# Performance work log

Hardware: AMD Instinct MI355X
Metric: run time of the kernel (lower is better)

The kernel has to match this reference:

```python
import jax, jax.numpy as jnp
import numpy as np

N_CELLS, N_GENES = 10000, 4000
CELL_F, GENE_F = 2000, 50
HID, LAT, NCLUST = 256, 64, 20
N_EDGES = 640000
ALPHA = 1.0


def _lin(key, fan_in, fan_out):
    k1, k2 = jax.random.split(key)
    bound = 1.0 / np.sqrt(fan_in)
    w = jax.random.uniform(k1, (fan_in, fan_out), jnp.float32, -bound, bound)
    b = jax.random.uniform(k2, (fan_out,), jnp.float32, -bound, bound)
    return w, b


def setup_inputs() -> dict:
    key = jax.random.key(0)
    ks = jax.random.split(key, 20)
    inp = {
        'cell_x': jax.random.normal(ks[0], (N_CELLS, CELL_F), jnp.float32),
        'gene_x': jax.random.normal(ks[1], (N_GENES, GENE_F), jnp.float32),
        'edge_row': jax.random.randint(ks[2], (N_EDGES,), 0, N_CELLS),
        'edge_col': jax.random.randint(ks[3], (N_EDGES,), 0, N_GENES),
        'edge_val': jax.random.uniform(ks[4], (N_EDGES,), jnp.float32),
    }
    # layer 0: cell_in=CELL_F, gene_in=GENE_F -> HID
    inp['l0_cs_w'], inp['l0_cs_b'] = _lin(ks[5], CELL_F, HID)
    inp['l0_cn_w'], inp['l0_cn_b'] = _lin(ks[6], GENE_F, HID)
    inp['l0_gs_w'], inp['l0_gs_b'] = _lin(ks[7], GENE_F, HID)
    inp['l0_gn_w'], inp['l0_gn_b'] = _lin(ks[8], CELL_F, HID)
    # layer 1: HID -> HID
    inp['l1_cs_w'], inp['l1_cs_b'] = _lin(ks[9], HID, HID)
    inp['l1_cn_w'], inp['l1_cn_b'] = _lin(ks[10], HID, HID)
    inp['l1_gs_w'], inp['l1_gs_b'] = _lin(ks[11], HID, HID)
    inp['l1_gn_w'], inp['l1_gn_b'] = _lin(ks[12], HID, HID)
    # latent heads and decoders
    inp['cl_w'], inp['cl_b'] = _lin(ks[13], HID, LAT)
    inp['gl_w'], inp['gl_b'] = _lin(ks[14], HID, LAT)
    inp['cd_w'], inp['cd_b'] = _lin(ks[15], LAT, N_GENES)
    inp['gd_w'], inp['gd_b'] = _lin(ks[16], LAT, N_CELLS)
    inp['centers'] = jax.random.normal(ks[17], (NCLUST, LAT), jnp.float32)
    return inp


def _bip_conv(cell_x, gene_x, er, ec, ev,
              cs_w, cs_b, cn_w, cn_b, gs_w, gs_b, gn_w, gn_b):
    # sparse adjacency matmul as gather + segment_sum over edge list
    cell_neigh = jax.ops.segment_sum(ev[:, None] * gene_x[ec], er,
                                     num_segments=cell_x.shape[0])
    gene_neigh = jax.ops.segment_sum(ev[:, None] * cell_x[er], ec,
                                     num_segments=gene_x.shape[0])
    cell_out = jax.nn.relu(cell_x @ cs_w + cs_b + cell_neigh @ cn_w + cn_b)
    gene_out = jax.nn.relu(gene_x @ gs_w + gs_b + gene_neigh @ gn_w + gn_b)
    return cell_out, gene_out


def reference(cell_x, gene_x, edge_row, edge_col, edge_val,
              l0_cs_w, l0_cs_b, l0_cn_w, l0_cn_b, l0_gs_w, l0_gs_b, l0_gn_w, l0_gn_b,
              l1_cs_w, l1_cs_b, l1_cn_w, l1_cn_b, l1_gs_w, l1_gs_b, l1_gn_w, l1_gn_b,
              cl_w, cl_b, gl_w, gl_b, cd_w, cd_b, gd_w, gd_b, centers):
    c, g = _bip_conv(cell_x, gene_x, edge_row, edge_col, edge_val,
                     l0_cs_w, l0_cs_b, l0_cn_w, l0_cn_b,
                     l0_gs_w, l0_gs_b, l0_gn_w, l0_gn_b)
    c, g = _bip_conv(c, g, edge_row, edge_col, edge_val,
                     l1_cs_w, l1_cs_b, l1_cn_w, l1_cn_b,
                     l1_gs_w, l1_gs_b, l1_gn_w, l1_gn_b)
    z_cells = c @ cl_w + cl_b
    z_genes = g @ gl_w + gl_b
    cell_recon = z_cells @ cd_w + cd_b
    gene_recon = z_genes @ gd_w + gd_b
    # Student-t cluster assignment (DEC)
    sq_dist = jnp.sum((z_cells[:, None, :] - centers[None, :, :]) ** 2, axis=-1)
    numerator = (1.0 + sq_dist / ALPHA) ** (-(ALPHA + 1.0) / 2.0)
    q = numerator / jnp.sum(numerator, axis=1, keepdims=True)
    return z_cells, z_genes, cell_recon, gene_recon, q
```

## Files before the change

kernel.cpp:

```cpp
#include <hip/hip_runtime.h>

#define N_CELLS 10000
#define N_GENES 4000
#define CELL_F  2000
#define CELL_FX 2112
#define GENE_F  50
#define GENE_FP 64
#define HID     256
#define LAT     64
#define NCLUST  20
#define N_EDGES 640000

typedef __attribute__((ext_vector_type(8))) short    bf16x8;
typedef __attribute__((ext_vector_type(8))) unsigned short u16x8;
typedef __attribute__((ext_vector_type(4))) float    f32x4;

__device__ __forceinline__ unsigned short f2bf(float f) {
    unsigned int u = __float_as_uint(f);
    unsigned int r = (u + 0x7FFFu + ((u >> 16) & 1u)) >> 16;
    return (unsigned short)r;
}
__device__ __forceinline__ float bf2f(unsigned short h) {
    return __uint_as_float(((unsigned int)h) << 16);
}

#define GLOAD_LDS16(gp, lp) __builtin_amdgcn_global_load_lds( \
    (const __attribute__((address_space(1))) void*)(gp), \
    (__attribute__((address_space(3))) void*)(lp), 16, 0, 0)

struct GemmDesc {
    const unsigned short *A, *BT;
    const float *bias;
    float *C;
    unsigned short *Cbf;
    int M, N, K;
    int gx, nwg, blk0;
    const float *bias2;
    unsigned short *Cbf2;
};
struct GemmArgs2 { GemmDesc d[2]; };
struct ScatArgs {
    const int *er, *ec; const float *ev;
    int *cur_c, *cur_g;
    int *ci; float *cv; int *gi; float *gv;
};

template<int TM, bool BIAS, bool WF32, bool WBF, bool TEPI, bool QTAIL, bool SCAT, bool RSPLIT>
__global__ __launch_bounds__(256)
void gemm_multi(GemmArgs2 ga, int gemm0, int qstart,
                const float* __restrict__ zq, const float* __restrict__ cent,
                float* __restrict__ qout, ScatArgs sa)
{
    constexpr int SMEM = (TM * 128 + 8192) > 16640 ? (TM * 128 + 8192) : 16640;
    __shared__ __align__(16) unsigned char smem[SMEM];
    unsigned short* As = (unsigned short*)smem;
    unsigned short* Bs = As + TM * 64;

    if (SCAT && (int)blockIdx.x < gemm0) {
        int e = blockIdx.x * 256 + threadIdx.x;
        int r = sa.er[e], c = sa.ec[e];
        float v = sa.ev[e];
        int pc = atomicAdd(&sa.cur_c[r], 1);
        sa.ci[pc] = c; sa.cv[pc] = v;
        int pg = atomicAdd(&sa.cur_g[c], 1);
        sa.gi[pg] = r; sa.gv[pg] = v;
        return;
    }

    if (QTAIL && (int)blockIdx.x >= qstart) {
        float* cs = (float*)smem;
        int tid = threadIdx.x;
        for (int l = tid; l < NCLUST * LAT; l += 256) cs[l] = cent[l];
        __syncthreads();
        int c = (blockIdx.x - qstart) * 256 + tid;
        if (c >= N_CELLS) return;
        float zr[LAT];
        #pragma unroll
        for (int k = 0; k < LAT; ++k) zr[k] = zq[(size_t)c * LAT + k];
        float num[NCLUST];
        float denom = 0.0f;
        for (int j = 0; j < NCLUST; ++j) {
            float d = 0.0f;
            #pragma unroll
            for (int k = 0; k < LAT; ++k) {
                float t = zr[k] - cs[j * LAT + k];
                d += t * t;
            }
            float n = 1.0f / (1.0f + d);
            num[j] = n;
            denom += n;
        }
        float inv = 1.0f / denom;
        for (int j = 0; j < NCLUST; ++j) qout[(size_t)c * NCLUST + j] = num[j] * inv;
        return;
    }

    int b = blockIdx.x;
    int p = (b >= ga.d[1].blk0) ? 1 : 0;
    const GemmDesc d = ga.d[p];
    int lin = b - d.blk0;
    int q8 = d.nwg >> 3, r8 = d.nwg & 7;
    int xcd = lin & 7, idx = lin >> 3;
    int wgid = (xcd < r8 ? xcd * (q8 + 1) : r8 * (q8 + 1) + (xcd - r8) * q8) + idx;
    int by = wgid / d.gx;
    int bx = wgid - by * d.gx;

    const int tid  = threadIdx.x;
    const int lane = tid & 63;
    const int w    = tid >> 6;
    const int cn   = lane & 15;
    const int rj   = lane >> 4;
    const int row0 = by * TM;
    const int col0 = bx * 64;

    constexpr int AI = TM / 32;
    constexpr int MF = TM / 64;

    size_t arow[AI];
    unsigned short* ldsA[AI];
    #pragma unroll
    for (int j = 0; j < AI; ++j) {
        int slot = (w * AI + j) * 64 + lane;
        int rs = slot >> 3, ss = slot & 7, cs = ss ^ (rs & 7);
        arow[j] = (size_t)min(row0 + rs, d.M - 1) * d.K + cs * 8;
        ldsA[j] = As + (w * AI + j) * 512;
    }
    const int sb0 = (w * 2) * 64 + lane;
    const int sb1 = sb0 + 64;
    const int rb0 = sb0 >> 3, cb0 = (sb0 & 7) ^ (rb0 & 7);
    const int rb1 = sb1 >> 3, cb1 = (sb1 & 7) ^ (rb1 & 7);
    const size_t brow0 = (size_t)(col0 + rb0) * d.K + cb0 * 8;
    const size_t brow1 = (size_t)(col0 + rb1) * d.K + cb1 * 8;
    unsigned short* ldsB = Bs + (w * 2) * 512;

    int aoff0[MF], aoff1[MF];
    #pragma unroll
    for (int mf = 0; mf < MF; ++mf) {
        int rA = w * (TM / 4) + mf * 16 + cn, swA = rA & 7, abase = rA * 64;
        aoff0[mf] = abase + ((rj)     ^ swA) * 8;
        aoff1[mf] = abase + ((rj + 4) ^ swA) * 8;
    }

    f32x4 acc[MF][4] = {};

    for (int kt = 0; kt < d.K; kt += 64) {
        #pragma unroll
        for (int j = 0; j < AI; ++j) GLOAD_LDS16(d.A + arow[j] + kt, ldsA[j]);
        GLOAD_LDS16(d.BT + brow0 + kt, ldsB);
        GLOAD_LDS16(d.BT + brow1 + kt, ldsB + 512);
        __syncthreads();
        bf16x8 a0[MF], a1[MF];
        #pragma unroll
        for (int mf = 0; mf < MF; ++mf) {
            a0[mf] = *(const bf16x8*)&As[aoff0[mf]];
            a1[mf] = *(const bf16x8*)&As[aoff1[mf]];
        }
        #pragma unroll
        for (int f = 0; f < 4; ++f) {
            int rB = f * 16 + cn, swB = rB & 7, bb = rB * 64;
            bf16x8 b0 = *(const bf16x8*)&Bs[bb + ((rj)     ^ swB) * 8];
            bf16x8 b1 = *(const bf16x8*)&Bs[bb + ((rj + 4) ^ swB) * 8];
            #pragma unroll
            for (int mf = 0; mf < MF; ++mf) {
                acc[mf][f] = __builtin_amdgcn_mfma_f32_16x16x32_bf16(a0[mf], b0, acc[mf][f], 0, 0, 0);
                acc[mf][f] = __builtin_amdgcn_mfma_f32_16x16x32_bf16(a1[mf], b1, acc[mf][f], 0, 0, 0);
            }
        }
        __syncthreads();
    }

    if (TEPI) {
        float* Cs = (float*)smem;
        __syncthreads();
        #pragma unroll
        for (int f = 0; f < 4; ++f)
            #pragma unroll
            for (int j = 0; j < 4; ++j)
                Cs[(w * 16 + rj * 4 + j) * 65 + f * 16 + cn] = acc[0][f][j];
        __syncthreads();
        #pragma unroll
        for (int i = 0; i < 4; ++i) {
            int slot = tid + i * 256;
            int rr = slot >> 4, c4 = (slot & 15) * 4;
            int gr = row0 + rr, gc = col0 + c4;
            if (gr < d.M && gc < d.N) {
                const float* cp = &Cs[rr * 65 + c4];
                float4 bv = BIAS ? *(const float4*)&d.bias[gc] : float4{0, 0, 0, 0};
                float4 v;
                v.x = cp[0] + bv.x; v.y = cp[1] + bv.y;
                v.z = cp[2] + bv.z; v.w = cp[3] + bv.w;
                *(float4*)&d.C[(size_t)gr * d.N + gc] = v;
            }
        }
    } else if (RSPLIT) {
        #pragma unroll
        for (int mf = 0; mf < MF; ++mf) {
            #pragma unroll
            for (int f = 0; f < 4; ++f) {
                int col = col0 + f * 16 + cn;
                #pragma unroll
                for (int j = 0; j < 4; ++j) {
                    int r = row0 + w * (TM / 4) + mf * 16 + rj * 4 + j;
                    if (r < d.M) {
                        float val = acc[mf][f][j];
                        if (col < 256) {
                            val += d.bias[col] + d.bias2[col];
                            d.Cbf[(size_t)r * 256 + col] = f2bf(fmaxf(val, 0.0f));
                        } else {
                            d.Cbf2[(size_t)r * 256 + (col - 256)] = f2bf(val);
                        }
                    }
                }
            }
        }
    } else {
        #pragma unroll
        for (int mf = 0; mf < MF; ++mf) {
            #pragma unroll
            for (int f = 0; f < 4; ++f) {
                int col = col0 + f * 16 + cn;
                if (col >= d.N) continue;
                float bv = BIAS ? d.bias[col] : 0.0f;
                #pragma unroll
                for (int j = 0; j < 4; ++j) {
                    int r = row0 + w * (TM / 4) + mf * 16 + rj * 4 + j;
                    if (r < d.M) {
                        float val = acc[mf][f][j] + bv;
                        if (WF32) d.C[(size_t)r * d.N + col] = val;
                        if (WBF)  d.Cbf[(size_t)r * d.N + col] = f2bf(val);
                    }
                }
            }
        }
    }
}

__global__ __launch_bounds__(256)
void rawgather_kernel(const int* __restrict__ ptr, const int* __restrict__ nbr,
                      const float* __restrict__ val,
                      const unsigned short* __restrict__ gx,
                      unsigned short* __restrict__ cellx)
{
    int w = threadIdx.x >> 6, lane = threadIdx.x & 63;
    int r = blockIdx.x * 4 + w;
    int s = ptr[r], e = ptr[r + 1];
    int g = lane >> 4, sub = lane & 15;
    const ushort4* gx4 = (const ushort4*)gx;
    float4 acc = {0.0f, 0.0f, 0.0f, 0.0f};
    for (int base = s; base < e; base += 16) {
        int nb = 0; float vb = 0.0f;
        if (lane < 16 && base + lane < e) { nb = nbr[base + lane]; vb = val[base + lane]; }
        #pragma unroll
        for (int jj = 0; jj < 4; ++jj) {
            int ei = jj * 4 + g;
            int j  = __shfl(nb, ei);
            float v = __shfl(vb, ei);
            ushort4 a = gx4[(size_t)j * 16 + sub];
            acc.x += v * bf2f(a.x);
            acc.y += v * bf2f(a.y);
            acc.z += v * bf2f(a.z);
            acc.w += v * bf2f(a.w);
        }
    }
    acc.x += __shfl_xor(acc.x, 16); acc.x += __shfl_xor(acc.x, 32);
    acc.y += __shfl_xor(acc.y, 16); acc.y += __shfl_xor(acc.y, 32);
    acc.z += __shfl_xor(acc.z, 16); acc.z += __shfl_xor(acc.z, 32);
    acc.w += __shfl_xor(acc.w, 16); acc.w += __shfl_xor(acc.w, 32);
    if (lane < 16) {
        ushort4 o;
        o.x = f2bf(acc.x); o.y = f2bf(acc.y); o.z = f2bf(acc.z); o.w = f2bf(acc.w);
        ((ushort4*)(cellx + (size_t)r * CELL_FX + 2048))[sub] = o;
    }
}

struct PackDesc {
    const float* W1; const float* W2; const float* W3; unsigned short* BT;
    int Kr, Kp, N1, N2, Np, xb, blk0;
};
struct PackArgs { PackDesc d[8]; };

#define CNT_BLK   2500
#define CVTC_BLK  10000
#define CVTG_BLK  125
#define PACK_BLK0 (CNT_BLK + CVTC_BLK + CVTG_BLK)

__global__ __launch_bounds__(256)
void prep_kernel(const int* __restrict__ er, const int* __restrict__ ec,
                 int* __restrict__ cnt_c, int* __restrict__ cnt_g,
                 const float* __restrict__ cell_x, unsigned short* __restrict__ cellx_bf,
                 const float* __restrict__ gene_x, unsigned short* __restrict__ genex_bf,
                 PackArgs pa)
{
    __shared__ float tile[32][33];
    int b = blockIdx.x;
    int tid = threadIdx.x;
    if (b < CNT_BLK) {
        int e = b * 256 + tid;
        atomicAdd(&cnt_c[er[e]], 1);
        atomicAdd(&cnt_g[ec[e]], 1);
        return;
    }
    if (b < CNT_BLK + CVTC_BLK) {
        int row = b - CNT_BLK;
        int col = tid * 8;
        u16x8 v = {0, 0, 0, 0, 0, 0, 0, 0};
        if (col < CELL_F) {
            const float* src = cell_x + (size_t)row * CELL_F + col;
            float4 f0 = *(const float4*)src;
            float4 f1 = *(const float4*)(src + 4);
            v[0] = f2bf(f0.x); v[1] = f2bf(f0.y); v[2] = f2bf(f0.z); v[3] = f2bf(f0.w);
            v[4] = f2bf(f1.x); v[5] = f2bf(f1.y); v[6] = f2bf(f1.z); v[7] = f2bf(f1.w);
        }
        ((u16x8*)(cellx_bf + (size_t)row * CELL_FX))[tid] = v;
        return;
    }
    if (b < PACK_BLK0) {
        int idx = (b - CNT_BLK - CVTC_BLK) * 256 + tid;
        int row = idx >> 3, c8 = idx & 7;
        int col = c8 * 8;
        u16x8 v = {0, 0, 0, 0, 0, 0, 0, 0};
        #pragma unroll
        for (int j = 0; j < 8; ++j)
            if (col + j < GENE_F) v[j] = f2bf(gene_x[(size_t)row * GENE_F + col + j]);
        ((u16x8*)(genex_bf + (size_t)row * GENE_FP))[c8] = v;
        return;
    }
    int pb = b;
    int p = 0;
    #pragma unroll
    for (int i = 1; i < 8; ++i) if (pb >= pa.d[i].blk0) p = i;
    const PackDesc d = pa.d[p];
    int local = pb - d.blk0;
    int kb = local % d.xb, nb = local / d.xb;
    int k0 = kb * 32, n0 = nb * 32;
    int tx = tid & 31, ty = tid >> 5;
    #pragma unroll
    for (int yy = 0; yy < 4; ++yy) {
        int k = k0 + ty + yy * 8;
        int n = n0 + tx;
        float v = 0.0f;
        if (k < d.Kr) {
            if (n < d.N1) v = d.W1[(size_t)k * d.N1 + n];
            else if (n < d.N1 + d.N2) v = d.W2[(size_t)k * d.N2 + (n - d.N1)];
        } else if (d.W3 && k >= 2048) {
            int kk = k - 2048;
            if (kk < GENE_F && n < HID) v = d.W3[(size_t)kk * HID + n];
        }
        tile[ty + yy * 8][tx] = v;
    }
    __syncthreads();
    #pragma unroll
    for (int yy = 0; yy < 4; ++yy) {
        int n = n0 + ty + yy * 8;
        int k = k0 + tx;
        if (n < d.Np)
            d.BT[(size_t)n * d.Kp + k] = f2bf(tile[tx][ty + yy * 8]);
    }
}

__global__ __launch_bounds__(1024)
void scan2_kernel(const int* __restrict__ cnt_c, int* __restrict__ ptr_c, int* __restrict__ cur_c,
                  const int* __restrict__ cnt_g, int* __restrict__ ptr_g, int* __restrict__ cur_g)
{
    const int* cnt = blockIdx.x ? cnt_g : cnt_c;
    int* ptr = blockIdx.x ? ptr_g : ptr_c;
    int* cur = blockIdx.x ? cur_g : cur_c;
    int  n   = blockIdx.x ? N_GENES : N_CELLS;
    __shared__ int part[1024];
    int t = threadIdx.x;
    int chunk = (n + 1023) / 1024;
    int lo = t * chunk, hi = min(lo + chunk, n);
    int s = 0;
    for (int i = lo; i < hi; ++i) s += cnt[i];
    part[t] = s;
    __syncthreads();
    #pragma unroll
    for (int off = 1; off < 1024; off <<= 1) {
        int v = (t >= off) ? part[t - off] : 0;
        __syncthreads();
        part[t] += v;
        __syncthreads();
    }
    if (t == 1023) ptr[n] = part[1023];
    int run = part[t] - s;
    for (int i = lo; i < hi; ++i) { ptr[i] = run; cur[i] = run; run += cnt[i]; }
}

struct AggSide {
    const int *ptr, *nbr; const float *val;
    const unsigned short *src, *pre;
    const float *b1, *b2;
    unsigned short *out;
    int srcRow4, srcOff4, preRow;
};
struct AggArgs { AggSide s[2]; int nc; };

__global__ __launch_bounds__(256)
void agg2_kernel(AggArgs aa)
{
    __shared__ __align__(16) float red[4][256];
    int b = blockIdx.x;
    int side = (b >= aa.nc) ? 1 : 0;
    const AggSide S = aa.s[side];
    int r = side ? b - aa.nc : b;
    int t = threadIdx.x;
    int w = t >> 6;
    int lane = t & 63;
    int s = S.ptr[r], e = S.ptr[r + 1];
    int n = e - s;
    int chunk = (n + 3) >> 2;
    int ws = s + w * chunk;
    int we = min(ws + chunk, e);
    const ushort4* src4 = (const ushort4*)S.src;
    float4 acc = {0.0f, 0.0f, 0.0f, 0.0f};
    for (int base = ws; base < we; base += 16) {
        int   nb = 0;
        float vb = 0.0f;
        if (lane < 16 && base + lane < we) {
            nb = S.nbr[base + lane];
            vb = S.val[base + lane];
        }
        #pragma unroll
        for (int j = 0; j < 16; ++j) {
            int   jj = __shfl(nb, j);
            float vv = __shfl(vb, j);
            ushort4 a = src4[(size_t)jj * S.srcRow4 + S.srcOff4 + lane];
            acc.x += vv * bf2f(a.x);
            acc.y += vv * bf2f(a.y);
            acc.z += vv * bf2f(a.z);
            acc.w += vv * bf2f(a.w);
        }
    }
    *(float4*)&red[w][lane * 4] = acc;
    __syncthreads();
    float x = red[0][t] + red[1][t] + red[2][t] + red[3][t]
            + bf2f(S.pre[(size_t)r * S.preRow + t]) + S.b1[t] + S.b2[t];
    S.out[(size_t)r * 256 + t] = f2bf(fmaxf(x, 0.0f));
}

extern "C" void kernel_launch(void* const* d_in, const int* in_sizes, int n_in,
                              void* d_out, int out_size, void* d_ws, size_t ws_size,
                              hipStream_t stream)
{
    const float* cell_x  = (const float*)d_in[0];
    const float* gene_x  = (const float*)d_in[1];
    const int*   er      = (const int*)d_in[2];
    const int*   ec      = (const int*)d_in[3];
    const float* ev      = (const float*)d_in[4];
    const float* l0_cs_w = (const float*)d_in[5];  const float* l0_cs_b = (const float*)d_in[6];
    const float* l0_cn_w = (const float*)d_in[7];  const float* l0_cn_b = (const float*)d_in[8];
    const float* l0_gs_w = (const float*)d_in[9];  const float* l0_gs_b = (const float*)d_in[10];
    const float* l0_gn_w = (const float*)d_in[11]; const float* l0_gn_b = (const float*)d_in[12];
    const float* l1_cs_w = (const float*)d_in[13]; const float* l1_cs_b = (const float*)d_in[14];
    const float* l1_cn_w = (const float*)d_in[15]; const float* l1_cn_b = (const float*)d_in[16];
    const float* l1_gs_w = (const float*)d_in[17]; const float* l1_gs_b = (const float*)d_in[18];
    const float* l1_gn_w = (const float*)d_in[19]; const float* l1_gn_b = (const float*)d_in[20];
    const float* cl_w = (const float*)d_in[21]; const float* cl_b = (const float*)d_in[22];
    const float* gl_w = (const float*)d_in[23]; const float* gl_b = (const float*)d_in[24];
    const float* cd_w = (const float*)d_in[25]; const float* cd_b = (const float*)d_in[26];
    const float* gd_w = (const float*)d_in[27]; const float* gd_b = (const float*)d_in[28];
    const float* centers = (const float*)d_in[29];

    float* out = (float*)d_out;
    float* z_cells    = out;
    float* z_genes    = out + 640000;
    float* cell_recon = out + 896000;
    float* gene_recon = out + 40896000;
    float* q          = out + 80896000;

    char* wsp = (char*)d_ws;
    auto alloc = [&](size_t bytes) -> void* {
        void* p = (void*)wsp;
        wsp += (bytes + 255) & ~(size_t)255;
        return p;
    };
    unsigned short* pre_c_bf = (unsigned short*)alloc((size_t)N_CELLS * 512 * 2);
    unsigned short* pre_g_bf = (unsigned short*)alloc((size_t)N_GENES * 512 * 2);
    unsigned short* c1_bf    = (unsigned short*)alloc((size_t)N_CELLS * 256 * 2);
    unsigned short* g1_bf    = (unsigned short*)alloc((size_t)N_GENES * 256 * 2);
    unsigned short* c2_bf    = (unsigned short*)alloc((size_t)N_CELLS * 256 * 2);
    unsigned short* g2_bf    = (unsigned short*)alloc((size_t)N_GENES * 256 * 2);
    unsigned short* zc_bf    = (unsigned short*)alloc((size_t)N_CELLS * 64 * 2);
    unsigned short* zg_bf    = (unsigned short*)alloc((size_t)N_GENES * 64 * 2);
    unsigned short* cellx_bf = (unsigned short*)alloc((size_t)N_CELLS * CELL_FX * 2);
    unsigned short* genex_bf = (unsigned short*)alloc((size_t)N_GENES * GENE_FP * 2);
    unsigned short* W0cT = (unsigned short*)alloc((size_t)512 * CELL_FX * 2);
    unsigned short* W0gT = (unsigned short*)alloc((size_t)256 * GENE_FP * 2);
    unsigned short* W1cT = (unsigned short*)alloc((size_t)512 * HID * 2);
    unsigned short* W1gT = (unsigned short*)alloc((size_t)512 * HID * 2);
    unsigned short* WzcT = (unsigned short*)alloc((size_t)64 * HID * 2);
    unsigned short* WzgT = (unsigned short*)alloc((size_t)64 * HID * 2);
    unsigned short* WdcT = (unsigned short*)alloc((size_t)4032 * 64 * 2);
    unsigned short* WdgT = (unsigned short*)alloc((size_t)10048 * 64 * 2);
    int* cnt_c = (int*)alloc((size_t)(N_CELLS + N_GENES) * 4);
    int* cnt_g = cnt_c + N_CELLS;
    int* ptr_c = (int*)alloc((size_t)(N_CELLS + 1) * 4);
    int* ptr_g = (int*)alloc((size_t)(N_GENES + 1) * 4);
    int* cur_c = (int*)alloc((size_t)N_CELLS * 4);
    int* cur_g = (int*)alloc((size_t)N_GENES * 4);
    int*   ci = (int*)alloc((size_t)N_EDGES * 4);
    float* cv = (float*)alloc((size_t)N_EDGES * 4);
    int*   gi = (int*)alloc((size_t)N_EDGES * 4);
    float* gv = (float*)alloc((size_t)N_EDGES * 4);
    unsigned short* pre_cgn_bf = c2_bf;
    unsigned short* pre_gs_bf  = g2_bf;

    hipMemsetAsync(cnt_c, 0, (size_t)(N_CELLS + N_GENES) * 4, stream);

    {
        PackArgs pa;
        auto set = [&](int i, const float* W1, const float* W2, const float* W3,
                       unsigned short* BT, int Kr, int Kp, int N1, int N2, int Np,
                       int blk0) -> int {
            int xb = Kp / 32, yb = Np / 32;
            pa.d[i] = {W1, W2, W3, BT, Kr, Kp, N1, N2, Np, xb, blk0};
            return blk0 + xb * yb;
        };
        int nb = PACK_BLK0;
        nb = set(0, l0_cs_w, l0_gn_w, l0_cn_w, W0cT, CELL_F, CELL_FX, HID, HID, 512, nb);
        nb = set(1, l0_gs_w, nullptr, nullptr, W0gT, GENE_F, GENE_FP, HID, 0, 256, nb);
        nb = set(2, l1_cs_w, l1_gn_w, nullptr, W1cT, HID, HID, HID, HID, 512, nb);
        nb = set(3, l1_gs_w, l1_cn_w, nullptr, W1gT, HID, HID, HID, HID, 512, nb);
        nb = set(4, cl_w, nullptr, nullptr, WzcT, HID, HID, LAT, 0, 64, nb);
        nb = set(5, gl_w, nullptr, nullptr, WzgT, HID, HID, LAT, 0, 64, nb);
        nb = set(6, cd_w, nullptr, nullptr, WdcT, LAT, LAT, N_GENES, 0, 4032, nb);
        nb = set(7, gd_w, nullptr, nullptr, WdgT, LAT, LAT, N_CELLS, 0, 10048, nb);
        prep_kernel<<<nb, 256, 0, stream>>>(er, ec, cnt_c, cnt_g,
                                            cell_x, cellx_bf, gene_x, genex_bf, pa);
    }

    scan2_kernel<<<2, 1024, 0, stream>>>(cnt_c, ptr_c, cur_c, cnt_g, ptr_g, cur_g);

    auto mkdesc = [](const unsigned short* A, const unsigned short* BT, const float* bias,
                     float* C, unsigned short* Cbf, int M, int N, int K, int TMv,
                     int blk0) -> GemmDesc {
        int gx = (N + 63) / 64, gy = (M + TMv - 1) / TMv;
        return {A, BT, bias, C, Cbf, M, N, K, gx, gx * gy, blk0, nullptr, nullptr};
    };
    ScatArgs sa0 = {er, ec, ev, cur_c, cur_g, ci, cv, gi, gv};
    ScatArgs saN = {};

    {
        GemmArgs2 ga;
        ga.d[0] = mkdesc(genex_bf, W0gT, nullptr, nullptr, pre_gs_bf, N_GENES, 256, GENE_FP, 128, CNT_BLK);
        ga.d[1] = ga.d[0]; ga.d[1].blk0 = 1 << 30;
        gemm_multi<128, false, false, true, false, false, true, false>
            <<<CNT_BLK + ga.d[0].nwg, 256, 0, stream>>>(
            ga, CNT_BLK, 1 << 30, nullptr, nullptr, nullptr, sa0);
    }

    rawgather_kernel<<<N_CELLS / 4, 256, 0, stream>>>(ptr_c, ci, cv, genex_bf, cellx_bf);

    {
        GemmArgs2 ga;
        ga.d[0] = mkdesc(cellx_bf, W0cT, l0_cs_b, nullptr, c1_bf, N_CELLS, 512, CELL_FX, 128, 0);
        ga.d[0].bias2 = l0_cn_b;
        ga.d[0].Cbf2  = pre_cgn_bf;
        ga.d[1] = ga.d[0]; ga.d[1].blk0 = 1 << 30;
        gemm_multi<128, false, false, false, false, false, false, true>
            <<<ga.d[0].nwg, 256, 0, stream>>>(
            ga, 0, 1 << 30, nullptr, nullptr, nullptr, saN);
    }

    {
        AggArgs aa;
        aa.nc = 0;
        aa.s[1] = {ptr_g, gi, gv, pre_cgn_bf, pre_gs_bf, l0_gs_b, l0_gn_b, g1_bf, 64, 0, 256};
        aa.s[0] = aa.s[1];
        agg2_kernel<<<N_GENES, 256, 0, stream>>>(aa);
    }

    {
        GemmArgs2 ga;
        ga.d[0] = mkdesc(c1_bf, W1cT, nullptr, nullptr, pre_c_bf, N_CELLS, 512, HID, 128, 0);
        ga.d[1] = mkdesc(g1_bf, W1gT, nullptr, nullptr, pre_g_bf, N_GENES, 512, HID, 128,
                         ga.d[0].nwg);
        gemm_multi<128, false, false, true, false, false, false, false>
            <<<ga.d[1].blk0 + ga.d[1].nwg, 256, 0, stream>>>(
            ga, 0, 1 << 30, nullptr, nullptr, nullptr, saN);
    }

    {
        AggArgs aa;
        aa.nc = N_CELLS;
        aa.s[0] = {ptr_c, ci, cv, pre_g_bf, pre_c_bf, l1_cs_b, l1_cn_b, c2_bf, 128, 64, 512};
        aa.s[1] = {ptr_g, gi, gv, pre_c_bf, pre_g_bf, l1_gs_b, l1_gn_b, g2_bf, 128, 64, 512};
        agg2_kernel<<<N_CELLS + N_GENES, 256, 0, stream>>>(aa);
    }

    {
        GemmArgs2 ga;
        ga.d[0] = mkdesc(c2_bf, WzcT, cl_b, z_cells, zc_bf, N_CELLS, LAT, HID, 64, 0);
        ga.d[1] = mkdesc(g2_bf, WzgT, gl_b, z_genes, zg_bf, N_GENES, LAT, HID, 64, ga.d[0].nwg);
        gemm_multi<64, true, true, true, false, false, false, false>
            <<<ga.d[1].blk0 + ga.d[1].nwg, 256, 0, stream>>>(
            ga, 0, 1 << 30, nullptr, nullptr, nullptr, saN);
    }

    {
        GemmArgs2 ga;
        ga.d[0] = mkdesc(zc_bf, WdcT, cd_b, cell_recon, nullptr, N_CELLS, N_GENES, LAT, 64, 0);
        ga.d[1] = mkdesc(zg_bf, WdgT, gd_b, gene_recon, nullptr, N_GENES, N_CELLS, LAT, 64,
                         ga.d[0].nwg);
        int qstart = ga.d[1].blk0 + ga.d[1].nwg;
        int qblocks = (N_CELLS + 255) / 256;
        gemm_multi<64, true, true, false, true, true, false, false>
            <<<qstart + qblocks, 256, 0, stream>>>(
            ga, 0, qstart, z_cells, centers, q, saN);
    }
}
```

Before: 436.4 us.

## Aggregate raw layer-1 features before GEMM and fuse self/neighbor weights along K

Layer 1 now aggregates the raw hidden features into the second half of a concatenated [h | neighbor-sum] buffer. It then runs one GEMM with K=512 against stacked self and neighbor weights, with bias and ReLU fused into the epilogue. Before, it projected features to a 512-wide output first and aggregated the projected half afterwards. This removes the separate read of the precomputed self term in the aggregation and halves the GEMM output width. In exchange the GEMM reads a wider A matrix, and neighbor sums are rounded to bf16 before the matmul rather than after.

Measured after the change: 421.2 us (median of 2 runs). 1.04x faster.

```diff
diff --git a/kernel.cpp b/kernel.cpp
--- a/kernel.cpp
+++ b/kernel.cpp
@@ -37,6 +37,7 @@
     int gx, nwg, blk0;
     const float *bias2;
     unsigned short *Cbf2;
+    int ld1, ld2;
 };
 struct GemmArgs2 { GemmDesc d[2]; };
 struct ScatArgs {
@@ -198,6 +199,7 @@
             #pragma unroll
             for (int f = 0; f < 4; ++f) {
                 int col = col0 + f * 16 + cn;
+                if (col >= d.N) continue;
                 #pragma unroll
                 for (int j = 0; j < 4; ++j) {
                     int r = row0 + w * (TM / 4) + mf * 16 + rj * 4 + j;
@@ -205,9 +207,9 @@
                         float val = acc[mf][f][j];
                         if (col < 256) {
                             val += d.bias[col] + d.bias2[col];
-                            d.Cbf[(size_t)r * 256 + col] = f2bf(fmaxf(val, 0.0f));
+                            d.Cbf[(size_t)r * d.ld1 + col] = f2bf(fmaxf(val, 0.0f));
                         } else {
-                            d.Cbf2[(size_t)r * 256 + (col - 256)] = f2bf(val);
+                            d.Cbf2[(size_t)r * d.ld2 + (col - 256)] = f2bf(val);
                         }
                     }
                 }
@@ -275,7 +277,7 @@
 
 struct PackDesc {
     const float* W1; const float* W2; const float* W3; unsigned short* BT;
-    int Kr, Kp, N1, N2, Np, xb, blk0;
+    int Kr, Kp, N1, N2, Np, xb, blk0, kcat;
 };
 struct PackArgs { PackDesc d[8]; };
 
@@ -339,7 +341,11 @@
         int k = k0 + ty + yy * 8;
         int n = n0 + tx;
         float v = 0.0f;
-        if (k < d.Kr) {
+        if (d.kcat) {
+            if (n < d.Np)
+                v = (k < 256) ? d.W1[(size_t)k * d.N1 + n]
+                              : d.W2[(size_t)(k - 256) * d.N1 + n];
+        } else if (k < d.Kr) {
             if (n < d.N1) v = d.W1[(size_t)k * d.N1 + n];
             else if (n < d.N1 + d.N2) v = d.W2[(size_t)k * d.N2 + (n - d.N1)];
         } else if (d.W3 && k >= 2048) {
@@ -391,18 +397,14 @@
     const unsigned short *src, *pre;
     const float *b1, *b2;
     unsigned short *out;
-    int srcRow4, srcOff4, preRow;
+    int srcRow4, srcOff4, preRow, outLd;
 };
-struct AggArgs { AggSide s[2]; int nc; };
 
 __global__ __launch_bounds__(256)
-void agg2_kernel(AggArgs aa)
+void agg1_kernel(AggSide S)
 {
     __shared__ __align__(16) float red[4][256];
-    int b = blockIdx.x;
-    int side = (b >= aa.nc) ? 1 : 0;
-    const AggSide S = aa.s[side];
-    int r = side ? b - aa.nc : b;
+    int r = blockIdx.x;
     int t = threadIdx.x;
     int w = t >> 6;
     int lane = t & 63;
@@ -435,7 +437,57 @@
     __syncthreads();
     float x = red[0][t] + red[1][t] + red[2][t] + red[3][t]
             + bf2f(S.pre[(size_t)r * S.preRow + t]) + S.b1[t] + S.b2[t];
-    S.out[(size_t)r * 256 + t] = f2bf(fmaxf(x, 0.0f));
+    S.out[(size_t)r * S.outLd + t] = f2bf(fmaxf(x, 0.0f));
+}
+
+struct NsSide {
+    const int *ptr, *nbr; const float *val;
+    const unsigned short *src;
+    unsigned short *out;
+    int srcRow4, srcOff4, outLd, outOff;
+};
+struct NsArgs { NsSide s[2]; int n0; };
+
+__global__ __launch_bounds__(256)
+void neighsum_kernel(NsArgs na)
+{
+    __shared__ __align__(16) float red[4][256];
+    int b = blockIdx.x;
+    int side = (b >= na.n0) ? 1 : 0;
+    const NsSide S = na.s[side];
+    int r = side ? b - na.n0 : b;
+    int t = threadIdx.x;
+    int w = t >> 6;
+    int lane = t & 63;
+    int s = S.ptr[r], e = S.ptr[r + 1];
+    int n = e - s;
+    int chunk = (n + 3) >> 2;
+    int ws = s + w * chunk;
+    int we = min(ws + chunk, e);
+    const ushort4* src4 = (const ushort4*)S.src;
+    float4 acc = {0.0f, 0.0f, 0.0f, 0.0f};
+    for (int base = ws; base < we; base += 16) {
+        int   nb = 0;
+        float vb = 0.0f;
+        if (lane < 16 && base + lane < we) {
+            nb = S.nbr[base + lane];
+            vb = S.val[base + lane];
+        }
+        #pragma unroll
+        for (int j = 0; j < 16; ++j) {
+            int   jj = __shfl(nb, j);
+            float vv = __shfl(vb, j);
+            ushort4 a = src4[(size_t)jj * S.srcRow4 + S.srcOff4 + lane];
+            acc.x += vv * bf2f(a.x);
+            acc.y += vv * bf2f(a.y);
+            acc.z += vv * bf2f(a.z);
+            acc.w += vv * bf2f(a.w);
+        }
+    }
+    *(float4*)&red[w][lane * 4] = acc;
+    __syncthreads();
+    float x = red[0][t] + red[1][t] + red[2][t] + red[3][t];
+    S.out[(size_t)r * S.outLd + S.outOff + t] = f2bf(x);
 }
 
 extern "C" void kernel_launch(void* const* d_in, const int* in_sizes, int n_in,
@@ -474,10 +526,10 @@
         wsp += (bytes + 255) & ~(size_t)255;
         return p;
     };
-    unsigned short* pre_c_bf = (unsigned short*)alloc((size_t)N_CELLS * 512 * 2);
-    unsigned short* pre_g_bf = (unsigned short*)alloc((size_t)N_GENES * 512 * 2);
-    unsigned short* c1_bf    = (unsigned short*)alloc((size_t)N_CELLS * 256 * 2);
-    unsigned short* g1_bf    = (unsigned short*)alloc((size_t)N_GENES * 256 * 2);
+    unsigned short* c1x_bf   = (unsigned short*)alloc((size_t)N_CELLS * 512 * 2);
+    unsigned short* g1x_bf   = (unsigned short*)alloc((size_t)N_GENES * 512 * 2);
+    unsigned short* pre_gs_bf  = (unsigned short*)alloc((size_t)N_GENES * 256 * 2);
+    unsigned short* pre_cgn_bf = (unsigned short*)alloc((size_t)N_CELLS * 256 * 2);
     unsigned short* c2_bf    = (unsigned short*)alloc((size_t)N_CELLS * 256 * 2);
     unsigned short* g2_bf    = (unsigned short*)alloc((size_t)N_GENES * 256 * 2);
     unsigned short* zc_bf    = (unsigned short*)alloc((size_t)N_CELLS * 64 * 2);
@@ -486,8 +538,8 @@
     unsigned short* genex_bf = (unsigned short*)alloc((size_t)N_GENES * GENE_FP * 2);
     unsigned short* W0cT = (unsigned short*)alloc((size_t)512 * CELL_FX * 2);
     unsigned short* W0gT = (unsigned short*)alloc((size_t)256 * GENE_FP * 2);
-    unsigned short* W1cT = (unsigned short*)alloc((size_t)512 * HID * 2);
-    unsigned short* W1gT = (unsigned short*)alloc((size_t)512 * HID * 2);
+    unsigned short* W1cT = (unsigned short*)alloc((size_t)256 * 512 * 2);
+    unsigned short* W1gT = (unsigned short*)alloc((size_t)256 * 512 * 2);
     unsigned short* WzcT = (unsigned short*)alloc((size_t)64 * HID * 2);
     unsigned short* WzgT = (unsigned short*)alloc((size_t)64 * HID * 2);
     unsigned short* WdcT = (unsigned short*)alloc((size_t)4032 * 64 * 2);
@@ -502,8 +554,6 @@
     float* cv = (float*)alloc((size_t)N_EDGES * 4);
     int*   gi = (int*)alloc((size_t)N_EDGES * 4);
     float* gv = (float*)alloc((size_t)N_EDGES * 4);
-    unsigned short* pre_cgn_bf = c2_bf;
-    unsigned short* pre_gs_bf  = g2_bf;
 
     hipMemsetAsync(cnt_c, 0, (size_t)(N_CELLS + N_GENES) * 4, stream);
 
@@ -511,20 +561,20 @@
         PackArgs pa;
         auto set = [&](int i, const float* W1, const float* W2, const float* W3,
                        unsigned short* BT, int Kr, int Kp, int N1, int N2, int Np,
-                       int blk0) -> int {
+                       int kcat, int blk0) -> int {
             int xb = Kp / 32, yb = Np / 32;
-            pa.d[i] = {W1, W2, W3, BT, Kr, Kp, N1, N2, Np, xb, blk0};
+            pa.d[i] = {W1, W2, W3, BT, Kr, Kp, N1, N2, Np, xb, blk0, kcat};
             return blk0 + xb * yb;
         };
         int nb = PACK_BLK0;
-        nb = set(0, l0_cs_w, l0_gn_w, l0_cn_w, W0cT, CELL_F, CELL_FX, HID, HID, 512, nb);
-        nb = set(1, l0_gs_w, nullptr, nullptr, W0gT, GENE_F, GENE_FP, HID, 0, 256, nb);
-        nb = set(2, l1_cs_w, l1_gn_w, nullptr, W1cT, HID, HID, HID, HID, 512, nb);
-        nb = set(3, l1_gs_w, l1_cn_w, nullptr, W1gT, HID, HID, HID, HID, 512, nb);
-        nb = set(4, cl_w, nullptr, nullptr, WzcT, HID, HID, LAT, 0, 64, nb);
-        nb = set(5, gl_w, nullptr, nullptr, WzgT, HID, HID, LAT, 0, 64, nb);
-        nb = set(6, cd_w, nullptr, nullptr, WdcT, LAT, LAT, N_GENES, 0, 4032, nb);
-        nb = set(7, gd_w, nullptr, nullptr, WdgT, LAT, LAT, N_CELLS, 0, 10048, nb);
+        nb = set(0, l0_cs_w, l0_gn_w, l0_cn_w, W0cT, CELL_F, CELL_FX, HID, HID, 512, 0, nb);
+        nb = set(1, l0_gs_w, nullptr, nullptr, W0gT, GENE_F, GENE_FP, HID, 0, 256, 0, nb);
+        nb = set(2, l1_cs_w, l1_cn_w, nullptr, W1cT, 512, 512, HID, 0, 256, 1, nb);
+        nb = set(3, l1_gs_w, l1_gn_w, nullptr, W1gT, 512, 512, HID, 0, 256, 1, nb);
+        nb = set(4, cl_w, nullptr, nullptr, WzcT, HID, HID, LAT, 0, 64, 0, nb);
+        nb = set(5, gl_w, nullptr, nullptr, WzgT, HID, HID, LAT, 0, 64, 0, nb);
+        nb = set(6, cd_w, nullptr, nullptr, WdcT, LAT, LAT, N_GENES, 0, 4032, 0, nb);
+        nb = set(7, gd_w, nullptr, nullptr, WdgT, LAT, LAT, N_CELLS, 0, 10048, 0, nb);
         prep_kernel<<<nb, 256, 0, stream>>>(er, ec, cnt_c, cnt_g,
                                             cell_x, cellx_bf, gene_x, genex_bf, pa);
     }
@@ -535,7 +585,7 @@
                      float* C, unsigned short* Cbf, int M, int N, int K, int TMv,
                      int blk0) -> GemmDesc {
         int gx = (N + 63) / 64, gy = (M + TMv - 1) / TMv;
-        return {A, BT, bias, C, Cbf, M, N, K, gx, gx * gy, blk0, nullptr, nullptr};
+        return {A, BT, bias, C, Cbf, M, N, K, gx, gx * gy, blk0, nullptr, nullptr, 0, 0};
     };
     ScatArgs sa0 = {er, ec, ev, cur_c, cur_g, ci, cv, gi, gv};
     ScatArgs saN = {};
@@ -553,9 +603,10 @@
 
     {
         GemmArgs2 ga;
-        ga.d[0] = mkdesc(cellx_bf, W0cT, l0_cs_b, nullptr, c1_bf, N_CELLS, 512, CELL_FX, 128, 0);
+        ga.d[0] = mkdesc(cellx_bf, W0cT, l0_cs_b, nullptr, c1x_bf, N_CELLS, 512, CELL_FX, 128, 0);
         ga.d[0].bias2 = l0_cn_b;
         ga.d[0].Cbf2  = pre_cgn_bf;
+        ga.d[0].ld1 = 512; ga.d[0].ld2 = 256;
         ga.d[1] = ga.d[0]; ga.d[1].blk0 = 1 << 30;
         gemm_multi<128, false, false, false, false, false, false, true>
             <<<ga.d[0].nwg, 256, 0, stream>>>(
@@ -563,29 +614,29 @@
     }
 
     {
-        AggArgs aa;
-        aa.nc = 0;
-        aa.s[1] = {ptr_g, gi, gv, pre_cgn_bf, pre_gs_bf, l0_gs_b, l0_gn_b, g1_bf, 64, 0, 256};
-        aa.s[0] = aa.s[1];
-        agg2_kernel<<<N_GENES, 256, 0, stream>>>(aa);
+        AggSide S = {ptr_g, gi, gv, pre_cgn_bf, pre_gs_bf, l0_gs_b, l0_gn_b,
+                     g1x_bf, 64, 0, 256, 512};
+        agg1_kernel<<<N_GENES, 256, 0, stream>>>(S);
+    }
+
+    {
+        NsArgs na;
+        na.n0 = N_CELLS;
+        na.s[0] = {ptr_c, ci, cv, g1x_bf, c1x_bf, 128, 0, 512, 256};
+        na.s[1] = {ptr_g, gi, gv, c1x_bf, g1x_bf, 128, 0, 512, 256};
+        neighsum_kernel<<<N_CELLS + N_GENES, 256, 0, stream>>>(na);
     }
 
     {
         GemmArgs2 ga;
-        ga.d[0] = mkdesc(c1_bf, W1cT, nullptr, nullptr, pre_c_bf, N_CELLS, 512, HID, 128, 0);
-        ga.d[1] = mkdesc(g1_bf, W1gT, nullptr, nullptr, pre_g_bf, N_GENES, 512, HID, 128,
+        ga.d[0] = mkdesc(c1x_bf, W1cT, l1_cs_b, nullptr, c2_bf, N_CELLS, 256, 512, 128, 0);
+        ga.d[0].bias2 = l1_cn_b; ga.d[0].ld1 = 256;
+        ga.d[1] = mkdesc(g1x_bf, W1gT, l1_gs_b, nullptr, g2_bf, N_GENES, 256, 512, 128,
                          ga.d[0].nwg);
-        gemm_multi<128, false, false, true, false, false, false, false>
+        ga.d[1].bias2 = l1_gn_b; ga.d[1].ld1 = 256;
+        gemm_multi<128, false, false, false, false, false, false, true>
             <<<ga.d[1].blk0 + ga.d[1].nwg, 256, 0, stream>>>(
             ga, 0, 1 << 30, nullptr, nullptr, nullptr, saN);
-    }
-
-    {
-        AggArgs aa;
-        aa.nc = N_CELLS;
-        aa.s[0] = {ptr_c, ci, cv, pre_g_bf, pre_c_bf, l1_cs_b, l1_cn_b, c2_bf, 128, 64, 512};
-        aa.s[1] = {ptr_g, gi, gv, pre_c_bf, pre_g_bf, l1_gs_b, l1_gn_b, g2_bf, 128, 64, 512};
-        agg2_kernel<<<N_CELLS + N_GENES, 256, 0, stream>>>(aa);
     }
 
     {
```
